# Kernel optimization log

Hardware: AMD Instinct MI355X
Metric: run time of the kernel (lower is better)

Reference implementation:

```python
import jax, jax.numpy as jnp
import numpy as np

D = 256      # d_model
L = 2        # num_layers
N = 10000    # num_nodes
E = 160000   # num_edges (avg degree 16)
EPS = 1e-5


def _ln(h, g, b):
    m = jnp.mean(h, axis=-1, keepdims=True)
    v = jnp.mean(jnp.square(h - m), axis=-1, keepdims=True)
    return (h - m) / jnp.sqrt(v + EPS) * g + b


def _lrelu(h):
    return jnp.where(h > 0, h, 0.2 * h)


def setup_inputs() -> dict:
    key = jax.random.key(0)
    ks = jax.random.split(key, 24)
    p = lambda k, shape: (jax.random.normal(k, shape, dtype=jnp.float32) * 0.05)
    inp = {
        "edge_index": jax.random.randint(ks[0], (2, E), 0, N),
        "x": jax.random.normal(ks[1], (N, D), dtype=jnp.float32),
        # per-layer attention / FF params (torch Linear convention: W is [out, in])
        "Wq": p(ks[2], (L, D, D)), "bq": p(ks[3], (L, D)),
        "Wk": p(ks[4], (L, D, D)), "bk": p(ks[5], (L, D)),
        "Wv": p(ks[6], (L, D, D)), "bv": p(ks[7], (L, D)),
        "Wff": p(ks[8], (L, D, D)), "bff": p(ks[9], (L, D)),
        # LayerNorm params
        "ga": jnp.ones((L, D), jnp.float32), "ba": jnp.zeros((L, D), jnp.float32),
        "gf": jnp.ones((L, D), jnp.float32), "bf": jnp.zeros((L, D), jnp.float32),
        "gfin": jnp.ones((D,), jnp.float32), "bfin": jnp.zeros((D,), jnp.float32),
        # head MLP
        "W3": p(ks[10], (3 * D, D)), "b3": p(ks[11], (3 * D,)),
        "W4": p(ks[12], (3 * D, 3 * D)), "b4": p(ks[13], (3 * D,)),
        "W5": p(ks[14], (D, 3 * D)), "b5": p(ks[15], (D,)),
        "Wvec": p(ks[16], (1, D)), "bvec": p(ks[17], (1,)),
    }
    return inp


def reference(edge_index, x, Wq, bq, Wk, bk, Wv, bv, Wff, bff,
              ga, ba, gf, bf, gfin, bfin, W3, b3, W4, b4, W5, b5, Wvec, bvec):
    num_nodes = x.shape[0]
    src = edge_index[0]  # [E]
    dst = edge_index[1]  # [E] (segment-softmax target)
    x_i = x[src]         # [E, D]
    query = x[dst]       # [E, D] (x_j)
    for i in range(Wq.shape[0]):
        q = query @ Wq[i].T + bq[i]            # [E, D]
        k = x_i @ Wk[i].T + bk[i]
        v = x_i @ Wv[i].T + bv[i]
        alpha = jnp.sum(q * k, axis=-1)        # [E]
        # segment softmax over dst
        amax = jax.ops.segment_max(alpha, dst, num_segments=num_nodes)
        e = jnp.exp(alpha - amax[dst])
        denom = jax.ops.segment_sum(e, dst, num_segments=num_nodes)
        attn = e / denom[dst]                  # [E]
        attn_out = q + attn[:, None] * v       # [E, D]
        query = _ln(attn_out, ga[i], ba[i])
        query = query @ Wff[i].T + bff[i]
    query = _lrelu(query)
    query = _ln(query, gf[0], bf[0])           # dropout = identity (eval)
    h = _lrelu(query @ W3.T + b3)              # [E, 3D]
    h = _lrelu(h @ W4.T + b4)                  # [E, 3D]
    h = h @ W5.T + b5                          # [E, D]
    h = _ln(h + query, gfin, bfin)
    adj_logits = (h @ Wvec.T + bvec)[:, 0]     # [E]
    return adj_logits
```

## Files before the change

kernel.cpp:

```cpp
#include <hip/hip_runtime.h>

#define D 256

typedef unsigned short u16;
typedef unsigned int u32;
typedef __attribute__((ext_vector_type(8))) short short8;
typedef __attribute__((ext_vector_type(4))) float f32x4;
typedef __attribute__((ext_vector_type(16))) float f32x16;

__device__ __forceinline__ float b2f(u16 u) {
    return __uint_as_float(((u32)u) << 16);
}
__device__ __forceinline__ u16 f2b(float f) {
    u32 u = __float_as_uint(f);
    return (u16)((u + 0x7FFFu + ((u >> 16) & 1u)) >> 16);
}
__device__ __forceinline__ u32 packf(float v) {
    u16 h = f2b(v);
    u16 l = f2b(v - b2f(h));
    return ((u32)h << 16) | l;
}
__device__ __forceinline__ float unpackf(u32 p) {
    return b2f((u16)(p >> 16)) + b2f((u16)(p & 0xffffu));
}
template<typename T> __device__ __forceinline__ float ld1(const T* p);
template<> __device__ __forceinline__ float ld1<u16>(const u16* p) { return b2f(*p); }
template<> __device__ __forceinline__ float ld1<u32>(const u32* p) { return unpackf(*p); }

__device__ __forceinline__ u32 f2ord(float f) {
    u32 b = __float_as_uint(f);
    return (b & 0x80000000u) ? ~b : (b | 0x80000000u);
}
__device__ __forceinline__ float ord2f(u32 u) {
    return (u & 0x80000000u) ? __uint_as_float(u & 0x7fffffffu)
                             : __uint_as_float(~u);
}

__device__ __forceinline__ float wred(float v) {
#pragma unroll
    for (int m = 32; m; m >>= 1) v += __shfl_xor(v, m);
    return v;
}

__device__ __forceinline__ void gl_lds16(const u16* g, u16* l) {
    __builtin_amdgcn_global_load_lds(
        (__attribute__((address_space(1))) void*)(u16*)g,
        (__attribute__((address_space(3))) void*)l, 16, 0, 0);
}

template<int ACT>
__global__ __launch_bounds__(512, 4)
void gemm2(const u16* __restrict__ A, const u16* __restrict__ Whi,
           const float* __restrict__ bias, u16* __restrict__ C,
           int M, int N, int K)
{
    __shared__ u16 sA[128 * 64];
    __shared__ u16 sWh[256 * 64];

    const int tid  = threadIdx.x;
    const int lane = tid & 63;
    const int w    = tid >> 6;
    const int wm   = (w & 1) * 64;
    const int wn   = (w >> 1) * 64;
    const int row0 = blockIdx.x * 128;
    const int col0 = blockIdx.y * 256;

    f32x16 acc[2][2];
#pragma unroll
    for (int i = 0; i < 2; ++i)
#pragma unroll
        for (int j = 0; j < 2; ++j)
#pragma unroll
            for (int r = 0; r < 16; ++r) acc[i][j][r] = 0.f;

    const int r31   = lane & 31;
    const int khalf = lane >> 5;
    const int skey  = (r31 & 7) ^ ((r31 >> 3) & 3);
    const int l8r = lane >> 3;
    const int l8c = lane & 7;

    for (int k0 = 0; k0 < K; k0 += 64) {
#pragma unroll
        for (int s = 0; s < 4; ++s) {
            const int rbase = w * 32 + s * 8;
            const int row = rbase + l8r;
            const int gch = l8c ^ (row & 7) ^ s;
            const size_t gW = (size_t)(col0 + row) * K + k0 + gch * 8;
            gl_lds16(Whi + gW, sWh + rbase * 64);
        }
#pragma unroll
        for (int s = 0; s < 2; ++s) {
            const int rbase = w * 16 + s * 8;
            const int row = rbase + l8r;
            const int gch = l8c ^ (row & 7) ^ ((w * 2 + s) & 3);
            const size_t gA = (size_t)(row0 + row) * K + k0 + gch * 8;
            gl_lds16(A + gA, sA + rbase * 64);
        }
        __syncthreads();

#pragma unroll
        for (int w4 = 0; w4 < 4; ++w4) {
            const int slot = ((w4 * 2 + khalf) ^ skey) * 8;
            short8 af[2], wf[2];
#pragma unroll
            for (int i = 0; i < 2; ++i)
                af[i] = *(const short8*)(sA + (wm + i * 32 + r31) * 64 + slot);
#pragma unroll
            for (int j = 0; j < 2; ++j)
                wf[j] = *(const short8*)(sWh + (wn + j * 32 + r31) * 64 + slot);
#pragma unroll
            for (int i = 0; i < 2; ++i)
#pragma unroll
                for (int j = 0; j < 2; ++j)
                    acc[i][j] = __builtin_amdgcn_mfma_f32_32x32x16_bf16(af[i], wf[j], acc[i][j], 0, 0, 0);
        }
        __syncthreads();
    }

#pragma unroll
    for (int j = 0; j < 2; ++j) {
        const int col = col0 + wn + j * 32 + r31;
        const float bb = bias[col];
#pragma unroll
        for (int i = 0; i < 2; ++i) {
            const int rowb = row0 + wm + i * 32 + 4 * khalf;
#pragma unroll
            for (int reg = 0; reg < 16; ++reg) {
                const int row = rowb + (reg & 3) + 8 * (reg >> 2);
                float v = acc[i][j][reg] + bb;
                if (ACT) v = v > 0.f ? v : 0.2f * v;
                C[(size_t)row * N + col] = f2b(v);
            }
        }
    }
}

__global__ __launch_bounds__(512, 4)
void gemm3w(const u16* __restrict__ Ah, const u16* __restrict__ Al,
            const u16* __restrict__ Wh_, const u16* __restrict__ Wl_,
            const float* __restrict__ bias,
            u16* __restrict__ Ch, u16* __restrict__ Cl,
            int M, int K)
{
    constexpr int N = 256;
    __shared__ u16 sAhi[128 * 32];
    __shared__ u16 sAlo[128 * 32];
    __shared__ u16 sWhi[256 * 32];
    __shared__ u16 sWlo[256 * 32];

    const int tid  = threadIdx.x;
    const int lane = tid & 63;
    const int w    = tid >> 6;
    const int wm   = (w & 1) * 64;
    const int wn   = (w >> 1) * 64;
    const int row0 = blockIdx.x * 128;

    f32x4 acc[4][4];
#pragma unroll
    for (int i = 0; i < 4; ++i)
#pragma unroll
        for (int j = 0; j < 4; ++j) acc[i][j] = (f32x4){0.f, 0.f, 0.f, 0.f};

    const int lrow = lane >> 2;
    const int gck  = (lane & 3) ^ ((lane >> 3) & 3);
    const int r15 = lane & 15;
    const int rck = ((lane >> 4) ^ ((r15 >> 1) & 3)) * 8;

    for (int k0 = 0; k0 < K; k0 += 32) {
#pragma unroll
        for (int s = 0; s < 2; ++s) {
            const int rbase = w * 32 + s * 16;
            const size_t gW = (size_t)(rbase + lrow) * K + k0 + gck * 8;
            gl_lds16(Wh_ + gW, sWhi + rbase * 32);
            gl_lds16(Wl_ + gW, sWlo + rbase * 32);
        }
        {
            const int rbase = w * 16;
            const size_t gA = (size_t)(row0 + rbase + lrow) * K + k0 + gck * 8;
            gl_lds16(Ah + gA, sAhi + rbase * 32);
            gl_lds16(Al + gA, sAlo + rbase * 32);
        }
        __syncthreads();

        short8 ah[4], al[4], wh[4], wl[4];
#pragma unroll
        for (int i = 0; i < 4; ++i) {
            const int offA = (wm + i * 16 + r15) * 32 + rck;
            ah[i] = *(const short8*)(sAhi + offA);
            al[i] = *(const short8*)(sAlo + offA);
        }
#pragma unroll
        for (int j = 0; j < 4; ++j) {
            const int offW = (wn + j * 16 + r15) * 32 + rck;
            wh[j] = *(const short8*)(sWhi + offW);
            wl[j] = *(const short8*)(sWlo + offW);
        }
#pragma unroll
        for (int i = 0; i < 4; ++i)
#pragma unroll
            for (int j = 0; j < 4; ++j) {
                acc[i][j] = __builtin_amdgcn_mfma_f32_16x16x32_bf16(ah[i], wh[j], acc[i][j], 0, 0, 0);
                acc[i][j] = __builtin_amdgcn_mfma_f32_16x16x32_bf16(ah[i], wl[j], acc[i][j], 0, 0, 0);
                acc[i][j] = __builtin_amdgcn_mfma_f32_16x16x32_bf16(al[i], wh[j], acc[i][j], 0, 0, 0);
            }
        __syncthreads();
    }

#pragma unroll
    for (int j = 0; j < 4; ++j) {
        const int col = wn + j * 16 + r15;
        const float bb = bias[col];
#pragma unroll
        for (int i = 0; i < 4; ++i) {
            const int rowb = row0 + wm + i * 16 + (lane >> 4) * 4;
#pragma unroll
            for (int r = 0; r < 4; ++r) {
                float v = acc[i][j][r] + bb;
                const size_t idx = (size_t)(rowb + r) * N + col;
                if (Cl) {
                    u16 hh = f2b(v);
                    Ch[idx] = hh;
                    Cl[idx] = f2b(v - b2f(hh));
                } else {
                    Ch[idx] = f2b(v);
                }
            }
        }
    }
}

__global__ __launch_bounds__(512, 4)
void gemm3n(const u16* __restrict__ Ah, const u16* __restrict__ Al,
            const u16* __restrict__ Whi, const u16* __restrict__ Wlo,
            const float* __restrict__ b0, const float* __restrict__ b1,
            const float* __restrict__ b2,
            u32* __restrict__ Cp, int M, int K)
{
    constexpr int N = 256;
    __shared__ u16 sAhi[128 * 32];
    __shared__ u16 sAlo[128 * 32];
    __shared__ u16 sWhi[256 * 32];
    __shared__ u16 sWlo[256 * 32];

    const int tid  = threadIdx.x;
    const int lane = tid & 63;
    const int w    = tid >> 6;
    const int wm   = (w & 1) * 64;
    const int wn   = (w >> 1) * 64;
    const int row0 = blockIdx.x * 128;
    const int y    = blockIdx.y;
    const float* bias = (y == 0) ? b0 : ((y == 1) ? b1 : b2);
    const u16* Wh = Whi + (size_t)y * N * K;
    const u16* Wl = Wlo + (size_t)y * N * K;
    u32* Cy = Cp + (size_t)y * M * N;

    f32x4 acc[4][4];
#pragma unroll
    for (int i = 0; i < 4; ++i)
#pragma unroll
        for (int j = 0; j < 4; ++j) acc[i][j] = (f32x4){0.f, 0.f, 0.f, 0.f};

    const int lrow = lane >> 2;
    const int gck  = (lane & 3) ^ ((lane >> 3) & 3);
    const int r15 = lane & 15;
    const int rck = ((lane >> 4) ^ ((r15 >> 1) & 3)) * 8;

    for (int k0 = 0; k0 < K; k0 += 32) {
#pragma unroll
        for (int s = 0; s < 2; ++s) {
            const int rbase = w * 32 + s * 16;
            const size_t gW = (size_t)(rbase + lrow) * K + k0 + gck * 8;
            gl_lds16(Wh + gW, sWhi + rbase * 32);
            gl_lds16(Wl + gW, sWlo + rbase * 32);
        }
        {
            const int rbase = w * 16;
            int arow = row0 + rbase + lrow;
            if (arow >= M) arow = M - 1;
            const size_t gA = (size_t)arow * K + k0 + gck * 8;
            gl_lds16(Ah + gA, sAhi + rbase * 32);
            gl_lds16(Al + gA, sAlo + rbase * 32);
        }
        __syncthreads();

        short8 ah[4], al[4], wh[4], wl[4];
#pragma unroll
        for (int i = 0; i < 4; ++i) {
            const int offA = (wm + i * 16 + r15) * 32 + rck;
            ah[i] = *(const short8*)(sAhi + offA);
            al[i] = *(const short8*)(sAlo + offA);
        }
#pragma unroll
        for (int j = 0; j < 4; ++j) {
            const int offW = (wn + j * 16 + r15) * 32 + rck;
            wh[j] = *(const short8*)(sWhi + offW);
            wl[j] = *(const short8*)(sWlo + offW);
        }
#pragma unroll
        for (int i = 0; i < 4; ++i)
#pragma unroll
            for (int j = 0; j < 4; ++j) {
                acc[i][j] = __builtin_amdgcn_mfma_f32_16x16x32_bf16(ah[i], wh[j], acc[i][j], 0, 0, 0);
                acc[i][j] = __builtin_amdgcn_mfma_f32_16x16x32_bf16(ah[i], wl[j], acc[i][j], 0, 0, 0);
                acc[i][j] = __builtin_amdgcn_mfma_f32_16x16x32_bf16(al[i], wh[j], acc[i][j], 0, 0, 0);
            }
        __syncthreads();
    }

#pragma unroll
    for (int j = 0; j < 4; ++j) {
        const int col = wn + j * 16 + r15;
        const float bb = bias[col];
#pragma unroll
        for (int i = 0; i < 4; ++i) {
            const int rowb = row0 + wm + i * 16 + (lane >> 4) * 4;
#pragma unroll
            for (int r = 0; r < 4; ++r) {
                const int row = rowb + r;
                if (row < M)
                    Cy[(size_t)row * N + col] = packf(acc[i][j][r] + bb);
            }
        }
    }
}

__global__ void pack_x(const float* __restrict__ x, u16* __restrict__ xh,
                       u16* __restrict__ xl, int n)
{
    int i = blockIdx.x * 256 + threadIdx.x;
    if (i < n) {
        float v = x[i];
        u16 h = f2b(v);
        xh[i] = h;
        xl[i] = f2b(v - b2f(h));
    }
}

struct WcvA { const float* s[23]; u16* h[23]; u16* l[23]; };
__global__ __launch_bounds__(256)
void wconv_all(WcvA a, int n)
{
    int i = blockIdx.x * 256 + threadIdx.x;
    if (i >= n) return;
    int r = i >> 16;
    int o = i & 65535;
    float v = a.s[r][o];
    u16 hh = f2b(v);
    a.h[r][o] = hh;
    if (a.l[r]) a.l[r][o] = f2b(v - b2f(hh));
}

__global__ void seg_init(u32* __restrict__ amax, float* __restrict__ denom, int n)
{
    int i = blockIdx.x * 256 + threadIdx.x;
    if (i < n) { amax[i] = 0u; denom[i] = 0.f; }
}

template<typename TQ, int MODE>
__global__ __launch_bounds__(256)
void attn_alpha(const int* __restrict__ src, const int* __restrict__ dst,
                const TQ* __restrict__ qn, const u32* __restrict__ kn,
                float* __restrict__ alpha, u32* __restrict__ amax, int E)
{
    int e = blockIdx.x * 4 + (threadIdx.x >> 6);
    int lane = threadIdx.x & 63;
    if (e >= E) return;
    int s = src[e], d = dst[e];
    const TQ* qp = MODE ? (qn + (size_t)e * D) : (qn + (size_t)d * D);
    const u32* kp = kn + (size_t)s * D;
    float dot = 0.f;
#pragma unroll
    for (int j = 0; j < 4; ++j)
        dot += ld1(qp + lane * 4 + j) * unpackf(kp[lane * 4 + j]);
    dot = wred(dot);
    if (lane == 0) {
        alpha[e] = dot;
        atomicMax(amax + d, f2ord(dot));
    }
}

__global__ void seg_exp(const int* __restrict__ dst, const float* __restrict__ alpha,
                        const u32* __restrict__ amax, float* __restrict__ ebuf,
                        float* __restrict__ denom, int E)
{
    int e = blockIdx.x * 256 + threadIdx.x;
    if (e >= E) return;
    int d = dst[e];
    float ex = expf(alpha[e] - ord2f(amax[d]));
    ebuf[e] = ex;
    atomicAdd(denom + d, ex);
}

template<typename TQ, int MODE>
__global__ __launch_bounds__(256)
void attn_out_ln(const int* __restrict__ src, const int* __restrict__ dst,
                 const TQ* __restrict__ qn, const u32* __restrict__ vn,
                 const float* __restrict__ ebuf, const float* __restrict__ denom,
                 const float* __restrict__ g, const float* __restrict__ bb,
                 u16* __restrict__ oh, u16* __restrict__ ol, int e0, int cm)
{
    int le = blockIdx.x * 4 + (threadIdx.x >> 6);
    int lane = threadIdx.x & 63;
    if (le >= cm) return;
    int ge = e0 + le;
    int s = src[ge], d = dst[ge];
    float attn = ebuf[ge] / denom[d];
    const TQ* qp = MODE ? (qn + (size_t)ge * D) : (qn + (size_t)d * D);
    const u32* vp = vn + (size_t)s * D;
    int d0 = lane * 4;
    float a0 = ld1(qp + d0 + 0) + attn * unpackf(vp[d0 + 0]);
    float a1 = ld1(qp + d0 + 1) + attn * unpackf(vp[d0 + 1]);
    float a2 = ld1(qp + d0 + 2) + attn * unpackf(vp[d0 + 2]);
    float a3 = ld1(qp + d0 + 3) + attn * unpackf(vp[d0 + 3]);
    float mean = wred(a0 + a1 + a2 + a3) * (1.f / D);
    float c0 = a0 - mean, c1 = a1 - mean, c2 = a2 - mean, c3 = a3 - mean;
    float var = wred(c0 * c0 + c1 * c1 + c2 * c2 + c3 * c3) * (1.f / D);
    float rstd = rsqrtf(var + 1e-5f);
    float t0 = c0 * rstd * g[d0 + 0] + bb[d0 + 0];
    float t1 = c1 * rstd * g[d0 + 1] + bb[d0 + 1];
    float t2 = c2 * rstd * g[d0 + 2] + bb[d0 + 2];
    float t3 = c3 * rstd * g[d0 + 3] + bb[d0 + 3];
    size_t base = (size_t)le * D + d0;
    ushort4 ph, pl;
    ph.x = f2b(t0); pl.x = f2b(t0 - b2f(ph.x));
    ph.y = f2b(t1); pl.y = f2b(t1 - b2f(ph.y));
    ph.z = f2b(t2); pl.z = f2b(t2 - b2f(ph.z));
    ph.w = f2b(t3); pl.w = f2b(t3 - b2f(ph.w));
    *(ushort4*)(oh + base) = ph;
    *(ushort4*)(ol + base) = pl;
}

__global__ __launch_bounds__(256)
void lrelu_ln(const u16* __restrict__ ih, const u16* __restrict__ il,
              const float* __restrict__ g, const float* __restrict__ bb,
              u16* __restrict__ out, int cm)
{
    int le = blockIdx.x * 4 + (threadIdx.x >> 6);
    int lane = threadIdx.x & 63;
    if (le >= cm) return;
    size_t base = (size_t)le * D + lane * 4;
    ushort4 xh = *(const ushort4*)(ih + base);
    ushort4 xl = *(const ushort4*)(il + base);
    float x0 = b2f(xh.x) + b2f(xl.x);
    float x1 = b2f(xh.y) + b2f(xl.y);
    float x2 = b2f(xh.z) + b2f(xl.z);
    float x3 = b2f(xh.w) + b2f(xl.w);
    float a0 = x0 > 0.f ? x0 : 0.2f * x0;
    float a1 = x1 > 0.f ? x1 : 0.2f * x1;
    float a2 = x2 > 0.f ? x2 : 0.2f * x2;
    float a3 = x3 > 0.f ? x3 : 0.2f * x3;
    float mean = wred(a0 + a1 + a2 + a3) * (1.f / D);
    float c0 = a0 - mean, c1 = a1 - mean, c2 = a2 - mean, c3 = a3 - mean;
    float var = wred(c0 * c0 + c1 * c1 + c2 * c2 + c3 * c3) * (1.f / D);
    float rstd = rsqrtf(var + 1e-5f);
    int d0 = lane * 4;
    ushort4 o;
    o.x = f2b(c0 * rstd * g[d0 + 0] + bb[d0 + 0]);
    o.y = f2b(c1 * rstd * g[d0 + 1] + bb[d0 + 1]);
    o.z = f2b(c2 * rstd * g[d0 + 2] + bb[d0 + 2]);
    o.w = f2b(c3 * rstd * g[d0 + 3] + bb[d0 + 3]);
    *(ushort4*)(out + base) = o;
}

__global__ __launch_bounds__(256)
void final_k(const u16* __restrict__ hp, const u16* __restrict__ qp,
             const float* __restrict__ gfin, const float* __restrict__ bfin,
             const float* __restrict__ wvec, const float* __restrict__ bvec,
             float* __restrict__ out, int e0, int cm)
{
    int le = blockIdx.x * 4 + (threadIdx.x >> 6);
    int lane = threadIdx.x & 63;
    if (le >= cm) return;
    size_t base = (size_t)le * D + lane * 4;
    ushort4 hv = *(const ushort4*)(hp + base);
    ushort4 qv = *(const ushort4*)(qp + base);
    float a0 = b2f(hv.x) + b2f(qv.x);
    float a1 = b2f(hv.y) + b2f(qv.y);
    float a2 = b2f(hv.z) + b2f(qv.z);
    float a3 = b2f(hv.w) + b2f(qv.w);
    float mean = wred(a0 + a1 + a2 + a3) * (1.f / D);
    float c0 = a0 - mean, c1 = a1 - mean, c2 = a2 - mean, c3 = a3 - mean;
    float var = wred(c0 * c0 + c1 * c1 + c2 * c2 + c3 * c3) * (1.f / D);
    float rstd = rsqrtf(var + 1e-5f);
    int d0 = lane * 4;
    float t0 = c0 * rstd * gfin[d0 + 0] + bfin[d0 + 0];
    float t1 = c1 * rstd * gfin[d0 + 1] + bfin[d0 + 1];
    float t2 = c2 * rstd * gfin[d0 + 2] + bfin[d0 + 2];
    float t3 = c3 * rstd * gfin[d0 + 3] + bfin[d0 + 3];
    float part = t0 * wvec[d0 + 0] + t1 * wvec[d0 + 1] +
                 t2 * wvec[d0 + 2] + t3 * wvec[d0 + 3];
    part = wred(part);
    if (lane == 0) out[e0 + le] = part + bvec[0];
}

extern "C" void kernel_launch(void* const* d_in, const int* in_sizes, int n_in,
                              void* d_out, int out_size, void* d_ws, size_t ws_size,
                              hipStream_t stream)
{
    const int*   ei   = (const int*)d_in[0];
    const float* x    = (const float*)d_in[1];
    const float* Wq   = (const float*)d_in[2];
    const float* bq   = (const float*)d_in[3];
    const float* Wk   = (const float*)d_in[4];
    const float* bk   = (const float*)d_in[5];
    const float* Wv   = (const float*)d_in[6];
    const float* bv   = (const float*)d_in[7];
    const float* Wff  = (const float*)d_in[8];
    const float* bff  = (const float*)d_in[9];
    const float* ga   = (const float*)d_in[10];
    const float* ba   = (const float*)d_in[11];
    const float* gf   = (const float*)d_in[12];
    const float* bf   = (const float*)d_in[13];
    const float* gfin = (const float*)d_in[14];
    const float* bfin = (const float*)d_in[15];
    const float* W3   = (const float*)d_in[16];
    const float* b3   = (const float*)d_in[17];
    const float* W4   = (const float*)d_in[18];
    const float* b4   = (const float*)d_in[19];
    const float* W5   = (const float*)d_in[20];
    const float* b5   = (const float*)d_in[21];
    const float* Wvec = (const float*)d_in[22];
    const float* bvec = (const float*)d_in[23];

    const int E  = in_sizes[0] / 2;
    const int Nn = in_sizes[1] / D;
    const int* src = ei;
    const int* dst = ei + E;

    char* base = (char*)d_ws;
    size_t off = 0;
    auto take = [&](size_t bytes) -> void* {
        off = (off + 255) & ~(size_t)255;
        void* r = base + off;
        off += bytes;
        return r;
    };
    u32*   nKV1 = (u32*)take((size_t)2 * Nn * D * 4);
    u16*   q1  = (u16*)take((size_t)E * D * 2);
    float* alpha = (float*)take((size_t)E * 4);
    float* ebuf  = (float*)take((size_t)E * 4);
    u32*   amax  = (u32*)take((size_t)Nn * 4);
    float* denom = (float*)take((size_t)Nn * 4);
    u16* wnh = (u16*)take((size_t)5 * D * D * 2);
    u16* wnl = (u16*)take((size_t)5 * D * D * 2);
    u16* wff0h = (u16*)take((size_t)D * D * 2); u16* wff0l = (u16*)take((size_t)D * D * 2);
    u16* wff1h = (u16*)take((size_t)D * D * 2); u16* wff1l = (u16*)take((size_t)D * D * 2);
    u16* wq1h  = (u16*)take((size_t)D * D * 2); u16* wq1l  = (u16*)take((size_t)D * D * 2);
    u16* w3h = (u16*)take((size_t)3 * D * D * 2);
    u16* w4h = (u16*)take((size_t)9 * D * D * 2);
    u16* w5h = (u16*)take((size_t)3 * D * D * 2);

    const size_t nodeB = (size_t)4 * Nn * D * 4;
    size_t rem = ws_size > off + 8192 ? ws_size - off - 8192 : 0;
    size_t cmA = rem / 4096;
    size_t cmB = rem > nodeB ? (rem - nodeB) / 2048 : 0;
    size_t CMs = (cmA * 2048 >= nodeB) ? cmA : cmB;
    CMs = (CMs / 128) * 128;
    if (CMs > (size_t)E) CMs = E;
    if (CMs > 32768) CMs = 32768;
    if (CMs < 128) CMs = 128;
    const int CM = (int)CMs;

    u16* cpl = (u16*)take((size_t)CM * D * 2 * 4);
    u16* c1h = cpl;
    u16* c1l = cpl + (size_t)CM * D;
    u16* c2h = cpl + (size_t)2 * CM * D;
    u16* c2l = cpl + (size_t)3 * CM * D;
    u16* c4  = cpl;
    u16* c5  = cpl + (size_t)3 * CM * D;
    size_t zoneB = (size_t)CM * 2048 > nodeB ? (size_t)CM * 2048 : nodeB;
    char* zone = (char*)take(zoneB);
    u16* c2n = (u16*)zone;
    u16* c3  = (u16*)(zone + (size_t)CM * D * 2);
    u16* xph = (u16*)zone;
    u16* xpl = xph + (size_t)Nn * D;
    u32* zQKV = (u32*)(zone + (size_t)Nn * D * 4);
    u32* zQ0 = zQKV;
    u32* zK0 = zQKV + (size_t)Nn * D;
    u32* zV0 = zQKV + (size_t)2 * Nn * D;
    u32* nK1 = nKV1;
    u32* nV1 = nKV1 + (size_t)Nn * D;

    dim3 blk(256);
    dim3 blk2(512);
    int gridSeg = (Nn + 255) / 256;
    int gridE4  = (E + 3) / 4;
    int gridE   = (E + 255) / 256;
    const int DD = D * D;

    pack_x<<<(Nn * D + 255) / 256, 256, 0, stream>>>(x, xph, xpl, Nn * D);

    WcvA wa;
    const float* ws_[23] = {Wq, Wk, Wv, Wk + DD, Wv + DD, Wff, Wff + DD, Wq + DD,
                            W3, W3 + DD, W3 + 2 * DD,
                            W4, W4 + DD, W4 + 2 * DD, W4 + 3 * DD, W4 + 4 * DD,
                            W4 + 5 * DD, W4 + 6 * DD, W4 + 7 * DD, W4 + 8 * DD,
                            W5, W5 + DD, W5 + 2 * DD};
    u16* wh_[23] = {wnh, wnh + DD, wnh + 2 * DD, wnh + 3 * DD, wnh + 4 * DD,
                    wff0h, wff1h, wq1h,
                    w3h, w3h + DD, w3h + 2 * DD,
                    w4h, w4h + DD, w4h + 2 * DD, w4h + 3 * DD, w4h + 4 * DD,
                    w4h + 5 * DD, w4h + 6 * DD, w4h + 7 * DD, w4h + 8 * DD,
                    w5h, w5h + DD, w5h + 2 * DD};
    u16* wl_[23] = {wnl, wnl + DD, wnl + 2 * DD, wnl + 3 * DD, wnl + 4 * DD,
                    wff0l, wff1l, wq1l,
                    nullptr, nullptr, nullptr,
                    nullptr, nullptr, nullptr, nullptr, nullptr,
                    nullptr, nullptr, nullptr, nullptr,
                    nullptr, nullptr, nullptr};
    for (int r = 0; r < 23; ++r) { wa.s[r] = ws_[r]; wa.h[r] = wh_[r]; wa.l[r] = wl_[r]; }
    wconv_all<<<(23 * DD) / 256, 256, 0, stream>>>(wa, 23 * DD);

    int gN = (Nn + 127) / 128;
    gemm3n<<<dim3(gN, 3), blk2, 0, stream>>>(xph, xpl, wnh, wnl, bq, bk, bv,
                                             zQKV, Nn, D);
    gemm3n<<<dim3(gN, 2), blk2, 0, stream>>>(xph, xpl, wnh + 3 * DD, wnl + 3 * DD,
                                             bk + D, bv + D, bv,
                                             nKV1, Nn, D);

    seg_init<<<gridSeg, 256, 0, stream>>>(amax, denom, Nn);
    attn_alpha<u32, 0><<<gridE4, blk, 0, stream>>>(src, dst, zQ0, zK0, alpha, amax, E);
    seg_exp<<<gridE, 256, 0, stream>>>(dst, alpha, amax, ebuf, denom, E);

    for (int e0 = 0; e0 < E; e0 += CM) {
        int cm = E - e0 < CM ? E - e0 : CM;
        int gE4 = (cm + 3) / 4;
        dim3 gD3(cm / 128);
        attn_out_ln<u32, 0><<<gE4, blk, 0, stream>>>(src, dst, zQ0, zV0, ebuf, denom,
                                                     ga, ba, c1h, c1l, e0, cm);
        gemm3w<<<gD3, blk2, 0, stream>>>(c1h, c1l, wff0h, wff0l, bff,
                                         c2h, c2l, cm, D);
        gemm3w<<<gD3, blk2, 0, stream>>>(c2h, c2l, wq1h, wq1l, bq + D,
                                         q1 + (size_t)e0 * D, (u16*)nullptr,
                                         cm, D);
    }

    seg_init<<<gridSeg, 256, 0, stream>>>(amax, denom, Nn);
    attn_alpha<u16, 1><<<gridE4, blk, 0, stream>>>(src, dst, q1, nK1, alpha, amax, E);
    seg_exp<<<gridE, 256, 0, stream>>>(dst, alpha, amax, ebuf, denom, E);

    for (int e0 = 0; e0 < E; e0 += CM) {
        int cm = E - e0 < CM ? E - e0 : CM;
        int gE4 = (cm + 3) / 4;
        dim3 gD3(cm / 128);
        dim3 g2a(cm / 128, (3 * D) / 256);
        dim3 g2b(cm / 128, D / 256);
        attn_out_ln<u16, 1><<<gE4, blk, 0, stream>>>(src, dst, q1, nV1, ebuf, denom,
                                                     ga + D, ba + D, c1h, c1l, e0, cm);
        gemm3w<<<gD3, blk2, 0, stream>>>(c1h, c1l, wff1h, wff1l, bff + D,
                                         c2h, c2l, cm, D);
        lrelu_ln<<<gE4, blk, 0, stream>>>(c2h, c2l, gf, bf, c2n, cm);
        gemm2<1><<<g2a, blk2, 0, stream>>>(c2n, w3h, b3, c3, cm, 3 * D, D);
        gemm2<1><<<g2a, blk2, 0, stream>>>(c3, w4h, b4, c4, cm, 3 * D, 3 * D);
        gemm2<0><<<g2b, blk2, 0, stream>>>(c4, w5h, b5, c5, cm, D, 3 * D);
        final_k<<<gE4, blk, 0, stream>>>(c5, c2n, gfin, bfin, Wvec, bvec,
                                         (float*)d_out, e0, cm);
    }
}
```

Measured before the change: 1.419 ms.

## Fold Wff0 into Wq1 and fuse lrelu+LayerNorm into FF GEMM epilogue

Precomputes the product Wq1·Wff0, with a combined bias, on the device so the layer-0 feed-forward GEMM and the layer-1 query GEMM become a single per-edge GEMM. It also fuses the leaky-ReLU and LayerNorm that follow the layer-1 feed-forward GEMM into that GEMM's epilogue, using a cross-wave shared-memory row reduction. This removes one full E×D×D three-pass GEMM, the separate lrelu_ln kernel, and the hi/lo intermediate buffer traffic. The trade-off is that the combined weight is rounded once as a hi/lo split, which changes the rounding behaviour. The variance is computed as E[x²]−m², which can lose precision.

```diff
diff --git a/kernel.cpp b/kernel.cpp
--- a/kernel.cpp
+++ b/kernel.cpp
@@ -135,12 +135,13 @@
     }
 }
 
+template<int LNF>
 __global__ __launch_bounds__(512, 4)
 void gemm3w(const u16* __restrict__ Ah, const u16* __restrict__ Al,
             const u16* __restrict__ Wh_, const u16* __restrict__ Wl_,
             const float* __restrict__ bias,
-            u16* __restrict__ Ch, u16* __restrict__ Cl,
-            int M, int K)
+            const float* __restrict__ lng, const float* __restrict__ lnb,
+            u16* __restrict__ Ch, int M, int K)
 {
     constexpr int N = 256;
     __shared__ u16 sAhi[128 * 32];
@@ -164,7 +165,8 @@
     const int lrow = lane >> 2;
     const int gck  = (lane & 3) ^ ((lane >> 3) & 3);
     const int r15 = lane & 15;
-    const int rck = ((lane >> 4) ^ ((r15 >> 1) & 3)) * 8;
+    const int hi16 = lane >> 4;
+    const int rck = (hi16 ^ ((r15 >> 1) & 3)) * 8;
 
     for (int k0 = 0; k0 < K; k0 += 32) {
 #pragma unroll
@@ -206,23 +208,71 @@
         __syncthreads();
     }
 
-#pragma unroll
-    for (int j = 0; j < 4; ++j) {
-        const int col = wn + j * 16 + r15;
-        const float bb = bias[col];
+    if (LNF == 0) {
+#pragma unroll
+        for (int j = 0; j < 4; ++j) {
+            const int col = wn + j * 16 + r15;
+            const float bb = bias[col];
+#pragma unroll
+            for (int i = 0; i < 4; ++i) {
+                const int rowb = row0 + wm + i * 16 + hi16 * 4;
+#pragma unroll
+                for (int r = 0; r < 4; ++r)
+                    Ch[(size_t)(rowb + r) * N + col] = f2b(acc[i][j][r] + bb);
+            }
+        }
+    } else {
+        float* red = (float*)sWhi;
+        const int cg = w >> 1;
 #pragma unroll
         for (int i = 0; i < 4; ++i) {
-            const int rowb = row0 + wm + i * 16 + (lane >> 4) * 4;
+            float s1[4] = {0.f, 0.f, 0.f, 0.f};
+            float s2[4] = {0.f, 0.f, 0.f, 0.f};
+#pragma unroll
+            for (int j = 0; j < 4; ++j) {
+                const float bb = bias[wn + j * 16 + r15];
+#pragma unroll
+                for (int r = 0; r < 4; ++r) {
+                    float v = acc[i][j][r] + bb;
+                    float a = v > 0.f ? v : 0.2f * v;
+                    s1[r] += a; s2[r] += a * a;
+                }
+            }
 #pragma unroll
             for (int r = 0; r < 4; ++r) {
-                float v = acc[i][j][r] + bb;
-                const size_t idx = (size_t)(rowb + r) * N + col;
-                if (Cl) {
-                    u16 hh = f2b(v);
-                    Ch[idx] = hh;
-                    Cl[idx] = f2b(v - b2f(hh));
-                } else {
-                    Ch[idx] = f2b(v);
+#pragma unroll
+                for (int m = 8; m; m >>= 1) {
+                    s1[r] += __shfl_xor(s1[r], m);
+                    s2[r] += __shfl_xor(s2[r], m);
+                }
+            }
+            if (r15 == 0) {
+#pragma unroll
+                for (int r = 0; r < 4; ++r) {
+                    const int lr = wm + i * 16 + hi16 * 4 + r;
+                    red[lr * 4 + cg] = s1[r];
+                    red[(128 + lr) * 4 + cg] = s2[r];
+                }
+            }
+        }
+        __syncthreads();
+#pragma unroll
+        for (int i = 0; i < 4; ++i) {
+#pragma unroll
+            for (int r = 0; r < 4; ++r) {
+                const int lr = wm + i * 16 + hi16 * 4 + r;
+                float m = (red[lr * 4 + 0] + red[lr * 4 + 1] +
+                           red[lr * 4 + 2] + red[lr * 4 + 3]) * (1.f / 256.f);
+                float e2 = (red[(128 + lr) * 4 + 0] + red[(128 + lr) * 4 + 1] +
+                            red[(128 + lr) * 4 + 2] + red[(128 + lr) * 4 + 3]) * (1.f / 256.f);
+                float rstd = rsqrtf(e2 - m * m + 1e-5f);
+                const size_t grow = (size_t)(row0 + lr);
+#pragma unroll
+                for (int j = 0; j < 4; ++j) {
+                    const int col = wn + j * 16 + r15;
+                    float v = acc[i][j][r] + bias[col];
+                    float a = v > 0.f ? v : 0.2f * v;
+                    Ch[grow * N + col] = f2b((a - m) * rstd * lng[col] + lnb[col]);
                 }
             }
         }
@@ -336,7 +386,7 @@
     }
 }
 
-struct WcvA { const float* s[23]; u16* h[23]; u16* l[23]; };
+struct WcvA { const float* s[21]; u16* h[21]; u16* l[21]; };
 __global__ __launch_bounds__(256)
 void wconv_all(WcvA a, int n)
 {
@@ -348,6 +398,28 @@
     u16 hh = f2b(v);
     a.h[r][o] = hh;
     if (a.l[r]) a.l[r][o] = f2b(v - b2f(hh));
+}
+
+__global__ __launch_bounds__(256)
+void wcomb(const float* __restrict__ Wq1, const float* __restrict__ Wff0,
+           const float* __restrict__ bff, const float* __restrict__ bq1,
+           u16* __restrict__ wch, u16* __restrict__ wcl, float* __restrict__ bc)
+{
+    const int o = blockIdx.x;
+    const int j = threadIdx.x;
+    const float* wq = Wq1 + (size_t)o * 256;
+    float s = 0.f;
+    for (int k = 0; k < 256; ++k)
+        s = fmaf(wq[k], Wff0[(size_t)k * 256 + j], s);
+    u16 h = f2b(s);
+    wch[(size_t)o * 256 + j] = h;
+    wcl[(size_t)o * 256 + j] = f2b(s - b2f(h));
+    float p = wq[j] * bff[j];
+    p = wred(p);
+    __shared__ float ps[4];
+    if ((j & 63) == 0) ps[j >> 6] = p;
+    __syncthreads();
+    if (j == 0) bc[o] = bq1[o] + ps[0] + ps[1] + ps[2] + ps[3];
 }
 
 __global__ void seg_init(u32* __restrict__ amax, float* __restrict__ denom, int n)
@@ -431,38 +503,6 @@
 }
 
 __global__ __launch_bounds__(256)
-void lrelu_ln(const u16* __restrict__ ih, const u16* __restrict__ il,
-              const float* __restrict__ g, const float* __restrict__ bb,
-              u16* __restrict__ out, int cm)
-{
-    int le = blockIdx.x * 4 + (threadIdx.x >> 6);
-    int lane = threadIdx.x & 63;
-    if (le >= cm) return;
-    size_t base = (size_t)le * D + lane * 4;
-    ushort4 xh = *(const ushort4*)(ih + base);
-    ushort4 xl = *(const ushort4*)(il + base);
-    float x0 = b2f(xh.x) + b2f(xl.x);
-    float x1 = b2f(xh.y) + b2f(xl.y);
-    float x2 = b2f(xh.z) + b2f(xl.z);
-    float x3 = b2f(xh.w) + b2f(xl.w);
-    float a0 = x0 > 0.f ? x0 : 0.2f * x0;
-    float a1 = x1 > 0.f ? x1 : 0.2f * x1;
-    float a2 = x2 > 0.f ? x2 : 0.2f * x2;
-    float a3 = x3 > 0.f ? x3 : 0.2f * x3;
-    float mean = wred(a0 + a1 + a2 + a3) * (1.f / D);
-    float c0 = a0 - mean, c1 = a1 - mean, c2 = a2 - mean, c3 = a3 - mean;
-    float var = wred(c0 * c0 + c1 * c1 + c2 * c2 + c3 * c3) * (1.f / D);
-    float rstd = rsqrtf(var + 1e-5f);
-    int d0 = lane * 4;
-    ushort4 o;
-    o.x = f2b(c0 * rstd * g[d0 + 0] + bb[d0 + 0]);
-    o.y = f2b(c1 * rstd * g[d0 + 1] + bb[d0 + 1]);
-    o.z = f2b(c2 * rstd * g[d0 + 2] + bb[d0 + 2]);
-    o.w = f2b(c3 * rstd * g[d0 + 3] + bb[d0 + 3]);
-    *(ushort4*)(out + base) = o;
-}
-
-__global__ __launch_bounds__(256)
 void final_k(const u16* __restrict__ hp, const u16* __restrict__ qp,
              const float* __restrict__ gfin, const float* __restrict__ bfin,
              const float* __restrict__ wvec, const float* __restrict__ bvec,
@@ -543,9 +583,10 @@
     float* denom = (float*)take((size_t)Nn * 4);
     u16* wnh = (u16*)take((size_t)5 * D * D * 2);
     u16* wnl = (u16*)take((size_t)5 * D * D * 2);
-    u16* wff0h = (u16*)take((size_t)D * D * 2); u16* wff0l = (u16*)take((size_t)D * D * 2);
     u16* wff1h = (u16*)take((size_t)D * D * 2); u16* wff1l = (u16*)take((size_t)D * D * 2);
-    u16* wq1h  = (u16*)take((size_t)D * D * 2); u16* wq1l  = (u16*)take((size_t)D * D * 2);
+    u16* wch = (u16*)take((size_t)D * D * 2);
+    u16* wcl = (u16*)take((size_t)D * D * 2);
+    float* bc = (float*)take((size_t)D * 4);
     u16* w3h = (u16*)take((size_t)3 * D * D * 2);
     u16* w4h = (u16*)take((size_t)9 * D * D * 2);
     u16* w5h = (u16*)take((size_t)3 * D * D * 2);
@@ -564,8 +605,6 @@
     u16* cpl = (u16*)take((size_t)CM * D * 2 * 4);
     u16* c1h = cpl;
     u16* c1l = cpl + (size_t)CM * D;
-    u16* c2h = cpl + (size_t)2 * CM * D;
-    u16* c2l = cpl + (size_t)3 * CM * D;
     u16* c4  = cpl;
     u16* c5  = cpl + (size_t)3 * CM * D;
     size_t zoneB = (size_t)CM * 2048 > nodeB ? (size_t)CM * 2048 : nodeB;
@@ -591,25 +630,25 @@
     pack_x<<<(Nn * D + 255) / 256, 256, 0, stream>>>(x, xph, xpl, Nn * D);
 
     WcvA wa;
-    const float* ws_[23] = {Wq, Wk, Wv, Wk + DD, Wv + DD, Wff, Wff + DD, Wq + DD,
+    const float* ws_[21] = {Wq, Wk, Wv, Wk + DD, Wv + DD, Wff + DD,
                             W3, W3 + DD, W3 + 2 * DD,
                             W4, W4 + DD, W4 + 2 * DD, W4 + 3 * DD, W4 + 4 * DD,
                             W4 + 5 * DD, W4 + 6 * DD, W4 + 7 * DD, W4 + 8 * DD,
                             W5, W5 + DD, W5 + 2 * DD};
-    u16* wh_[23] = {wnh, wnh + DD, wnh + 2 * DD, wnh + 3 * DD, wnh + 4 * DD,
-                    wff0h, wff1h, wq1h,
+    u16* wh_[21] = {wnh, wnh + DD, wnh + 2 * DD, wnh + 3 * DD, wnh + 4 * DD, wff1h,
                     w3h, w3h + DD, w3h + 2 * DD,
                     w4h, w4h + DD, w4h + 2 * DD, w4h + 3 * DD, w4h + 4 * DD,
                     w4h + 5 * DD, w4h + 6 * DD, w4h + 7 * DD, w4h + 8 * DD,
                     w5h, w5h + DD, w5h + 2 * DD};
-    u16* wl_[23] = {wnl, wnl + DD, wnl + 2 * DD, wnl + 3 * DD, wnl + 4 * DD,
-                    wff0l, wff1l, wq1l,
+    u16* wl_[21] = {wnl, wnl + DD, wnl + 2 * DD, wnl + 3 * DD, wnl + 4 * DD, wff1l,
                     nullptr, nullptr, nullptr,
                     nullptr, nullptr, nullptr, nullptr, nullptr,
                     nullptr, nullptr, nullptr, nullptr,
                     nullptr, nullptr, nullptr};
-    for (int r = 0; r < 23; ++r) { wa.s[r] = ws_[r]; wa.h[r] = wh_[r]; wa.l[r] = wl_[r]; }
-    wconv_all<<<(23 * DD) / 256, 256, 0, stream>>>(wa, 23 * DD);
+    for (int r = 0; r < 21; ++r) { wa.s[r] = ws_[r]; wa.h[r] = wh_[r]; wa.l[r] = wl_[r]; }
+    wconv_all<<<(21 * DD) / 256, 256, 0, stream>>>(wa, 21 * DD);
+
+    wcomb<<<256, 256, 0, stream>>>(Wq + DD, Wff, bff, bq + D, wch, wcl, bc);
 
     int gN = (Nn + 127) / 128;
     gemm3n<<<dim3(gN, 3), blk2, 0, stream>>>(xph, xpl, wnh, wnl, bq, bk, bv,
@@ -628,11 +667,9 @@
         dim3 gD3(cm / 128);
         attn_out_ln<u32, 0><<<gE4, blk, 0, stream>>>(src, dst, zQ0, zV0, ebuf, denom,
                                                      ga, ba, c1h, c1l, e0, cm);
-        gemm3w<<<gD3, blk2, 0, stream>>>(c1h, c1l, wff0h, wff0l, bff,
-                                         c2h, c2l, cm, D);
-        gemm3w<<<gD3, blk2, 0, stream>>>(c2h, c2l, wq1h, wq1l, bq + D,
-                                         q1 + (size_t)e0 * D, (u16*)nullptr,
-                                         cm, D);
+        gemm3w<0><<<gD3, blk2, 0, stream>>>(c1h, c1l, wch, wcl, bc,
+                                            (const float*)nullptr, (const float*)nullptr,
+                                            q1 + (size_t)e0 * D, cm, D);
     }
 
     seg_init<<<gridSeg, 256, 0, stream>>>(amax, denom, Nn);
@@ -647,9 +684,8 @@
         dim3 g2b(cm / 128, D / 256);
         attn_out_ln<u16, 1><<<gE4, blk, 0, stream>>>(src, dst, q1, nV1, ebuf, denom,
                                                      ga + D, ba + D, c1h, c1l, e0, cm);
-        gemm3w<<<gD3, blk2, 0, stream>>>(c1h, c1l, wff1h, wff1l, bff + D,
-                                         c2h, c2l, cm, D);
-        lrelu_ln<<<gE4, blk, 0, stream>>>(c2h, c2l, gf, bf, c2n, cm);
+        gemm3w<1><<<gD3, blk2, 0, stream>>>(c1h, c1l, wff1h, wff1l, bff + D,
+                                            gf, bf, c2n, cm, D);
         gemm2<1><<<g2a, blk2, 0, stream>>>(c2n, w3h, b3, c3, cm, 3 * D, D);
         gemm2<1><<<g2a, blk2, 0, stream>>>(c3, w4h, b4, c4, cm, 3 * D, 3 * D);
         gemm2<0><<<g2b, blk2, 0, stream>>>(c4, w5h, b5, c5, cm, D, 3 * D);
```

After: 1.251 ms. 1.13x faster.
